# Optimization experiments

Measured on AMD Instinct MI355X. Metric: run time of the kernel, lower is better.

## Reference

```python
import jax, jax.numpy as jnp
import numpy as np

NEG_BIG = -9e15
ALPHA = 0.2  # LeakyReLU negative slope


def setup_inputs() -> dict:
    key = jax.random.key(0)
    k1, k2, k3, k4 = jax.random.split(key, 4)
    B, N, F_in, F_out = 8, 2048, 128, 128
    h = jax.random.normal(k1, (B, N, F_in), dtype=jnp.float32)
    adj = jax.random.randint(k2, (B, N, N), 0, 2, dtype=jnp.int32)
    # xavier_uniform with gain=1.414
    def xavier(k, shape, gain=1.414):
        fan_in, fan_out = shape[0], shape[1]
        bound = gain * np.sqrt(6.0 / (fan_in + fan_out))
        return jax.random.uniform(k, shape, jnp.float32, -bound, bound)
    W = xavier(k3, (F_in, F_out))
    a = xavier(k4, (2 * F_out, 1))
    return {"h": h, "adj": adj, "W": W, "a": a}


def reference(h, adj, W, a):
    # h: [B,N,F_in], adj: [B,N,N], W: [F_in,F_out], a: [2*F_out,1]
    Wh = jnp.einsum('bnf,fo->bno', h, W)              # [B,N,F_out]
    F_out = W.shape[1]
    a1 = a[:F_out, 0]                                  # source part
    a2 = a[F_out:, 0]                                  # target part
    # additive attention decomposition: cat([Wh_i, Wh_j]) @ a == Wh_i@a1 + Wh_j@a2
    s1 = Wh @ a1                                       # [B,N]
    s2 = Wh @ a2                                       # [B,N]
    e = jax.nn.leaky_relu(s1[:, :, None] + s2[:, None, :], negative_slope=ALPHA)  # [B,N,N]
    e = jnp.where(adj > 0, e, NEG_BIG)
    attn = jax.nn.softmax(e, axis=-1)                  # [B,N,N]
    h_prime = jnp.einsum('bij,bjo->bio', attn, Wh)     # [B,N,F_out]
    return jax.nn.elu(h_prime)                         # concat=True path
```

## Files before the change

kernel.cpp:

```cpp
#include <hip/hip_runtime.h>
#include <hip/hip_bf16.h>
#include <string.h>

typedef __attribute__((ext_vector_type(8))) short short8;
typedef __attribute__((ext_vector_type(4))) float f32x4;
typedef __attribute__((ext_vector_type(4))) int int4v;
typedef __attribute__((ext_vector_type(4))) float float4v;
typedef __attribute__((ext_vector_type(4))) unsigned short ushort4v;

#define LOG2E 1.44269504088896340736f
#define NB 8
#define NN 2048
#define NF 128
#define PKW (NN / 64)
#define PKWORDS (NB * NN * PKW)

static __device__ inline unsigned short f2bf(float x) {
    __hip_bfloat16 b = __float2bfloat16(x);
    unsigned short u;
    __builtin_memcpy(&u, &b, 2);
    return u;
}
static __device__ inline float bf2f(unsigned short u) {
    union { unsigned u; float f; } v;
    v.u = ((unsigned)u) << 16;
    return v.f;
}

__global__ void k_sniff(const unsigned short* __restrict__ hraw,
                        int* __restrict__ flag) {
    int lane = threadIdx.x;
    int cnt = 0;
    for (int i = lane; i < 512; i += 64) {
        int e = (hraw[i] >> 7) & 0xFF;
        cnt += (e >= 102 && e <= 139) ? 1 : 0;
    }
#pragma unroll
    for (int off = 1; off < 64; off <<= 1) cnt += __shfl_xor(cnt, off);
    if (lane == 0) *flag = (cnt >= 450) ? 1 : 0;
}

__global__ __launch_bounds__(256) void k_pack(const int* __restrict__ adj,
                                              unsigned long long* __restrict__ pk) {
    const int wid = blockIdx.x * 4 + (threadIdx.x >> 6);
    const int lane = threadIdx.x & 63;
    const int wpw = PKWORDS / 4096;
    const size_t w0 = (size_t)wid * wpw;
    for (int i = 0; i < wpw; i += 4) {
        int v0 = adj[((w0 + i) << 6) | lane];
        int v1 = adj[((w0 + i + 1) << 6) | lane];
        int v2 = adj[((w0 + i + 2) << 6) | lane];
        int v3 = adj[((w0 + i + 3) << 6) | lane];
        unsigned long long m0 = __ballot(v0 > 0);
        unsigned long long m1 = __ballot(v1 > 0);
        unsigned long long m2 = __ballot(v2 > 0);
        unsigned long long m3 = __ballot(v3 > 0);
        if (lane == 0) {
            pk[w0 + i] = m0;
            pk[w0 + i + 1] = m1;
            pk[w0 + i + 2] = m2;
            pk[w0 + i + 3] = m3;
        }
    }
}

__global__ __launch_bounds__(256) void k_prep(const void* __restrict__ Wraw,
                                              const void* __restrict__ araw,
                                              const int* __restrict__ flag,
                                              short* __restrict__ WThi,
                                              short* __restrict__ WTlo,
                                              float* __restrict__ a1s,
                                              float* __restrict__ a2s) {
    const int bf16w = *flag;
    int idx = blockIdx.x * 256 + threadIdx.x;
    int k = idx >> 7, n = idx & 127;
    float x = bf16w ? bf2f(((const unsigned short*)Wraw)[idx])
                    : ((const float*)Wraw)[idx];
    unsigned short hi = f2bf(x);
    float lo = x - bf2f(hi);
    WThi[n * 128 + k] = (short)hi;
    WTlo[n * 128 + k] = (short)f2bf(lo);
    if (blockIdx.x == 0) {
        int i = threadIdx.x;
        float av = bf16w ? bf2f(((const unsigned short*)araw)[i])
                         : ((const float*)araw)[i];
        if (i < 128) a1s[i] = LOG2E * av;
        else a2s[i - 128] = LOG2E * av;
    }
}

__global__ __launch_bounds__(64) void k_gemm(const void* __restrict__ hraw,
                                             const int* __restrict__ flag,
                                             const short* __restrict__ WThi,
                                             const short* __restrict__ WTlo,
                                             const float* __restrict__ a1s,
                                             const float* __restrict__ a2s,
                                             float* __restrict__ s1,
                                             float* __restrict__ s2,
                                             short* __restrict__ WhT) {
    const int lane = threadIdx.x;
    const int lo = lane & 15, g = lane >> 4;
    const int i0 = blockIdx.x * 16;
    const int bf16w = *flag;

    short8 ahi[4], alo[4];
    if (bf16w) {
        const short* h16 = (const short*)hraw;
#pragma unroll
        for (int kc = 0; kc < 4; ++kc) {
            ahi[kc] = *(const short8*)(h16 + (size_t)(i0 + lo) * NF + kc * 32 + g * 8);
            alo[kc] = (short8){0, 0, 0, 0, 0, 0, 0, 0};
        }
    } else {
        const float* hf = (const float*)hraw;
#pragma unroll
        for (int kc = 0; kc < 4; ++kc) {
            const float* p = hf + (size_t)(i0 + lo) * NF + kc * 32 + g * 8;
            float4v x0 = *(const float4v*)(p);
            float4v x1 = *(const float4v*)(p + 4);
            short8 h8, l8;
#pragma unroll
            for (int q = 0; q < 4; ++q) {
                unsigned short u0 = f2bf(x0[q]);
                h8[q] = (short)u0;
                l8[q] = (short)f2bf(x0[q] - bf2f(u0));
                unsigned short u1 = f2bf(x1[q]);
                h8[q + 4] = (short)u1;
                l8[q + 4] = (short)f2bf(x1[q] - bf2f(u1));
            }
            ahi[kc] = h8;
            alo[kc] = l8;
        }
    }

    f32x4 acc[8];
#pragma unroll
    for (int t = 0; t < 8; ++t) acc[t] = (f32x4){0.f, 0.f, 0.f, 0.f};

#pragma unroll
    for (int t = 0; t < 8; ++t) {
#pragma unroll
        for (int kc = 0; kc < 4; ++kc) {
            const size_t boff = (size_t)(lo + 16 * t) * NF + kc * 32 + g * 8;
            short8 bhi = *(const short8*)(WThi + boff);
            short8 blo = *(const short8*)(WTlo + boff);
            acc[t] = __builtin_amdgcn_mfma_f32_16x16x32_bf16(ahi[kc], bhi, acc[t], 0, 0, 0);
            acc[t] = __builtin_amdgcn_mfma_f32_16x16x32_bf16(ahi[kc], blo, acc[t], 0, 0, 0);
            acc[t] = __builtin_amdgcn_mfma_f32_16x16x32_bf16(alo[kc], bhi, acc[t], 0, 0, 0);
        }
    }

    const int b = i0 >> 11;
    const int n0 = i0 & 2047;
    short* wt = WhT + (size_t)b * NF * NN;
#pragma unroll
    for (int t = 0; t < 8; ++t) {
        ushort4v u;
#pragma unroll
        for (int r = 0; r < 4; ++r) u[r] = f2bf(acc[t][r]);
        *(ushort4v*)(wt + (size_t)(lo + 16 * t) * NN + n0 + g * 4) = u;
    }

    float a1f[8], a2f[8];
#pragma unroll
    for (int t = 0; t < 8; ++t) {
        a1f[t] = a1s[lo + 16 * t];
        a2f[t] = a2s[lo + 16 * t];
    }
#pragma unroll
    for (int r = 0; r < 4; ++r) {
        float d1 = 0.f, d2 = 0.f;
#pragma unroll
        for (int t = 0; t < 8; ++t) {
            float w = acc[t][r];
            d1 += w * a1f[t];
            d2 += w * a2f[t];
        }
#pragma unroll
        for (int off = 1; off < 16; off <<= 1) {
            d1 += __shfl_xor(d1, off);
            d2 += __shfl_xor(d2, off);
        }
        if (lo == 0) {
            s1[i0 + g * 4 + r] = d1;
            s2[i0 + g * 4 + r] = d2;
        }
    }
}

__global__ __launch_bounds__(256) void k_s2max(const float* __restrict__ s2,
                                               float* __restrict__ s2m) {
    int b = blockIdx.x;
    float m = -1e30f;
    for (int i = threadIdx.x; i < NN; i += 256) m = fmaxf(m, s2[b * NN + i]);
#pragma unroll
    for (int off = 1; off < 64; off <<= 1) m = fmaxf(m, __shfl_xor(m, off));
    __shared__ float sm[4];
    if ((threadIdx.x & 63) == 0) sm[threadIdx.x >> 6] = m;
    __syncthreads();
    if (threadIdx.x == 0)
        s2m[b] = fmaxf(fmaxf(sm[0], sm[1]), fmaxf(sm[2], sm[3]));
}

template <int FINAL, int JS>
__global__ __launch_bounds__(256, 4) void k_attn3(const unsigned long long* __restrict__ pk,
                                                  const float* __restrict__ s1,
                                                  const float* __restrict__ s2,
                                                  const float* __restrict__ s2m,
                                                  const short* __restrict__ WhT,
                                                  const int* __restrict__ flag,
                                                  void* __restrict__ out,
                                                  float* __restrict__ pO,
                                                  float* __restrict__ pL) {
    const int tid = threadIdx.x;
    const int lane = tid & 63, wid = tid >> 6;
    const int lo = lane & 15, g = lane >> 4;
    const int gid = blockIdx.x;
    const int js = (JS > 1) ? (gid / (NB * 32)) : 0;
    const int rem = gid % (NB * 32);
    const int blk = rem & 31;
    const int b = rem >> 5;
    const int rowbase = blk * 64 + wid * 16;
    const int row = rowbase + lo;
    const int jbeg = js * (NN / JS);
    const int NT = (NN / JS) / 64;

    __shared__ short lds[2][128 * 64];

    const float s1v = s1[b * NN + row];
    const float tm = s1v + s2m[b];
    const float M = fmaxf(tm, 0.2f * tm);
    const unsigned long long* pkr = pk + (size_t)(b * NN + row) * PKW + (jbeg >> 6);
    const float* s2p = s2 + b * NN + jbeg;
    const short* vb = WhT + (size_t)b * NF * NN;

    const int sf = tid >> 1;
    const int sh = tid & 1;
    const short* sbase = vb + (size_t)sf * NN + jbeg + sh * 32;
    char* ldsc0 = (char*)&lds[0][0];
    char* ldsc1 = (char*)&lds[1][0];
    const unsigned swz = (unsigned)((sf & 7) << 4);
    const unsigned wb0 = (unsigned)(sf * 128 + sh * 64);
    const unsigned rsw = (unsigned)((lo & 7) << 4);

    f32x4 acc[8];
#pragma unroll
    for (int t = 0; t < 8; ++t) acc[t] = (f32x4){0.f, 0.f, 0.f, 0.f};
    float lsum = 0.f;

    {
        short8 s0 = *(const short8*)(sbase);
        short8 s1r = *(const short8*)(sbase + 8);
        short8 s2r = *(const short8*)(sbase + 16);
        short8 s3r = *(const short8*)(sbase + 24);
        *(short8*)(ldsc0 + ((wb0 + 0) ^ swz)) = s0;
        *(short8*)(ldsc0 + ((wb0 + 16) ^ swz)) = s1r;
        *(short8*)(ldsc0 + ((wb0 + 32) ^ swz)) = s2r;
        *(short8*)(ldsc0 + ((wb0 + 48) ^ swz)) = s3r;
    }
    unsigned long long mcur = pkr[0];
    float4v zc0 = *(const float4v*)(s2p + g * 8);
    float4v zc1 = *(const float4v*)(s2p + g * 8 + 4);
    float4v zc2 = *(const float4v*)(s2p + g * 8 + 32);
    float4v zc3 = *(const float4v*)(s2p + g * 8 + 36);
    __syncthreads();

    int cur = 0;
    for (int t = 0; t < NT; ++t) {
        short8 sn0, sn1, sn2, sn3;
        unsigned long long mnext = 0;
        float4v zn0, zn1, zn2, zn3;
        const bool more = (t + 1 < NT);
        if (more) {
            const short* sp = sbase + (t + 1) * 64;
            sn0 = *(const short8*)(sp);
            sn1 = *(const short8*)(sp + 8);
            sn2 = *(const short8*)(sp + 16);
            sn3 = *(const short8*)(sp + 24);
            mnext = pkr[t + 1];
            const float* zp = s2p + (t + 1) * 64 + g * 8;
            zn0 = *(const float4v*)(zp);
            zn1 = *(const float4v*)(zp + 4);
            zn2 = *(const float4v*)(zp + 32);
            zn3 = *(const float4v*)(zp + 36);
        }
        const char* cb = cur ? ldsc1 : ldsc0;

        const unsigned bits0 = (unsigned)(mcur >> (g * 8)) & 0xFFu;
        const unsigned bits1 = (unsigned)(mcur >> (32 + g * 8)) & 0xFFu;
        short8 pa0, pa1;
#pragma unroll
        for (int q = 0; q < 4; ++q) {
            float t0 = s1v + zc0[q];
            float e0 = fmaxf(t0, 0.2f * t0);
            float p0 = ((bits0 >> q) & 1u) ? exp2f(e0 - M) : 0.f;
            float t1 = s1v + zc1[q];
            float e1 = fmaxf(t1, 0.2f * t1);
            float p1 = ((bits0 >> (q + 4)) & 1u) ? exp2f(e1 - M) : 0.f;
            float t2 = s1v + zc2[q];
            float e2 = fmaxf(t2, 0.2f * t2);
            float p2 = ((bits1 >> q) & 1u) ? exp2f(e2 - M) : 0.f;
            float t3 = s1v + zc3[q];
            float e3 = fmaxf(t3, 0.2f * t3);
            float p3 = ((bits1 >> (q + 4)) & 1u) ? exp2f(e3 - M) : 0.f;
            pa0[q] = (short)f2bf(p0); pa0[q + 4] = (short)f2bf(p1);
            pa1[q] = (short)f2bf(p2); pa1[q + 4] = (short)f2bf(p3);
            lsum += p0 + p1 + p2 + p3;
        }

#pragma unroll
        for (int t8 = 0; t8 < 8; ++t8) {
            const unsigned rb0 = ((unsigned)((lo + 16 * t8) * 128 + g * 16)) ^ rsw;
            const unsigned rb1 = ((unsigned)((lo + 16 * t8) * 128 + 64 + g * 16)) ^ rsw;
            short8 v0 = *(const short8*)(cb + rb0);
            short8 v1 = *(const short8*)(cb + rb1);
            acc[t8] = __builtin_amdgcn_mfma_f32_16x16x32_bf16(pa0, v0, acc[t8], 0, 0, 0);
            acc[t8] = __builtin_amdgcn_mfma_f32_16x16x32_bf16(pa1, v1, acc[t8], 0, 0, 0);
        }

        if (more) {
            char* wb = cur ? ldsc0 : ldsc1;
            *(short8*)(wb + ((wb0 + 0) ^ swz)) = sn0;
            *(short8*)(wb + ((wb0 + 16) ^ swz)) = sn1;
            *(short8*)(wb + ((wb0 + 32) ^ swz)) = sn2;
            *(short8*)(wb + ((wb0 + 48) ^ swz)) = sn3;
            mcur = mnext;
            zc0 = zn0; zc1 = zn1; zc2 = zn2; zc3 = zn3;
        }
        __syncthreads();
        cur ^= 1;
    }

    lsum += __shfl_xor(lsum, 16);
    lsum += __shfl_xor(lsum, 32);

    if (FINAL) {
        const int bf16w = *flag;
        float inv[4];
#pragma unroll
        for (int r = 0; r < 4; ++r) inv[r] = 1.0f / __shfl(lsum, g * 4 + r);
#pragma unroll
        for (int t8 = 0; t8 < 8; ++t8) {
#pragma unroll
            for (int r = 0; r < 4; ++r) {
                float x = acc[t8][r] * inv[r];
                float y = (x > 0.f) ? x : (exp2f(x * LOG2E) - 1.0f);
                size_t oi = ((size_t)b * NN + rowbase + g * 4 + r) * NF + lo + 16 * t8;
                if (bf16w) ((__hip_bfloat16*)out)[oi] = __float2bfloat16(y);
                else ((float*)out)[oi] = y;
            }
        }
    } else {
        const int grp = b * 128 + blk * 4 + wid;
        float* po = pO + (size_t)(grp * JS + js) * (16 * NF);
#pragma unroll
        for (int t8 = 0; t8 < 8; ++t8)
#pragma unroll
            for (int r = 0; r < 4; ++r)
                po[(g * 4 + r) * NF + lo + 16 * t8] = acc[t8][r];
        if (g == 0) pL[(grp * JS + js) * 16 + lo] = lsum;
    }
}

__global__ __launch_bounds__(256) void k_combine(const float* __restrict__ pO,
                                                 const float* __restrict__ pL,
                                                 const int* __restrict__ flag,
                                                 void* __restrict__ out,
                                                 int jsplit) {
    int idx = blockIdx.x * 256 + threadIdx.x;
    if (idx >= NB * NN * NF) return;
    const int bf16w = *flag;
    int col = idx & 127;
    int rowg = idx >> 7;
    int r = rowg & 15;
    int grp = rowg >> 4;
    float o = 0.f, l = 0.f;
    for (int js = 0; js < jsplit; ++js) {
        int task = grp * jsplit + js;
        o += pO[(size_t)task * (16 * NF) + r * NF + col];
        l += pL[task * 16 + r];
    }
    float x = o / l;
    float y = (x > 0.f) ? x : (exp2f(x * LOG2E) - 1.0f);
    if (bf16w) ((__hip_bfloat16*)out)[idx] = __float2bfloat16(y);
    else ((float*)out)[idx] = y;
}

extern "C" void kernel_launch(void* const* d_in, const int* in_sizes, int n_in,
                              void* d_out, int out_size, void* d_ws, size_t ws_size,
                              hipStream_t stream) {
    const void* h = d_in[0];
    const int* adj = (const int*)d_in[1];
    const void* W = d_in[2];
    const void* a = d_in[3];

    char* ws = (char*)d_ws;
    auto align256 = [](size_t x) { return (x + 255) & ~(size_t)255; };
    size_t off = 0;
    int* flag = (int*)(ws + off);     off = align256(off + 256);
    short* WThi = (short*)(ws + off); off = align256(off + (size_t)128 * 128 * 2);
    short* WTlo = (short*)(ws + off); off = align256(off + (size_t)128 * 128 * 2);
    float* a1s = (float*)(ws + off);  off = align256(off + 128 * 4);
    float* a2s = (float*)(ws + off);  off = align256(off + 128 * 4);
    short* WhT = (short*)(ws + off);  off = align256(off + (size_t)NB * NF * NN * 2);
    float* s1 = (float*)(ws + off);   off = align256(off + (size_t)NB * NN * 4);
    float* s2 = (float*)(ws + off);   off = align256(off + (size_t)NB * NN * 4);
    float* s2m = (float*)(ws + off);  off = align256(off + (size_t)NB * 4);
    unsigned long long* pk = (unsigned long long*)(ws + off);
    off = align256(off + (size_t)PKWORDS * 8);

    const int ngrp = NB * 128;
    auto need = [&](int js) {
        return off + (size_t)ngrp * js * 16 * NF * 4 + 512 + (size_t)ngrp * js * 16 * 4;
    };
    int jsplit = (ws_size >= need(4)) ? 4 : ((ws_size >= need(2)) ? 2 : 1);
    float* pO = nullptr;
    float* pL = nullptr;
    if (jsplit > 1) {
        size_t pO_bytes = (size_t)ngrp * jsplit * 16 * NF * 4;
        size_t pL_bytes = (size_t)ngrp * jsplit * 16 * 4;
        pO = (float*)(ws + off); off = align256(off + pO_bytes);
        pL = (float*)(ws + off); off = align256(off + pL_bytes);
    }

    k_sniff<<<1, 64, 0, stream>>>((const unsigned short*)h, flag);
    k_pack<<<1024, 256, 0, stream>>>(adj, pk);
    k_prep<<<64, 256, 0, stream>>>(W, a, flag, WThi, WTlo, a1s, a2s);
    k_gemm<<<NB * NN / 16, 64, 0, stream>>>(h, flag, WThi, WTlo, a1s, a2s, s1, s2, WhT);
    k_s2max<<<NB, 256, 0, stream>>>(s2, s2m);
    if (jsplit == 4) {
        k_attn3<0, 4><<<NB * 32 * 4, 256, 0, stream>>>(pk, s1, s2, s2m, WhT, flag,
                                                       d_out, pO, pL);
    } else if (jsplit == 2) {
        k_attn3<0, 2><<<NB * 32 * 2, 256, 0, stream>>>(pk, s1, s2, s2m, WhT, flag,
                                                       d_out, pO, pL);
    } else {
        k_attn3<1, 1><<<NB * 32, 256, 0, stream>>>(pk, s1, s2, s2m, WhT, flag,
                                                   d_out, nullptr, nullptr);
    }
    if (jsplit > 1) {
        int nout = NB * NN * NF;
        k_combine<<<(nout + 255) / 256, 256, 0, stream>>>(pO, pL, flag, d_out, jsplit);
    }
}
```

Before: 87.86 us.

## Fuse pack and GEMM kernels, fold s2 max via atomics, stage masks in LDS

Drops the separate sniff and s2-max launches. Each wave now sniffs the dtype inline, and s2's max is folded into the GEMM through an order-preserving atomicMax key. The pack and GEMM work run in one heterogeneous launch, with the GEMM using four waves per block. The attention kernel preloads the packed mask and s2 into LDS and unrolls its double-buffer loop by two. The combine step is vectorised to float4. The aim is to cut launch count and global traffic in the inner loop, at the cost of more LDS use and atomics.

```diff
diff --git a/kernel.cpp b/kernel.cpp
--- a/kernel.cpp
+++ b/kernel.cpp
@@ -4,7 +4,6 @@
 
 typedef __attribute__((ext_vector_type(8))) short short8;
 typedef __attribute__((ext_vector_type(4))) float f32x4;
-typedef __attribute__((ext_vector_type(4))) int int4v;
 typedef __attribute__((ext_vector_type(4))) float float4v;
 typedef __attribute__((ext_vector_type(4))) unsigned short ushort4v;
 
@@ -14,6 +13,8 @@
 #define NF 128
 #define PKW (NN / 64)
 #define PKWORDS (NB * NN * PKW)
+#define NGEMMB 256
+#define NPACKB 1024
 
 static __device__ inline unsigned short f2bf(float x) {
     __hip_bfloat16 b = __float2bfloat16(x);
@@ -26,52 +27,35 @@
     v.u = ((unsigned)u) << 16;
     return v.f;
 }
-
-__global__ void k_sniff(const unsigned short* __restrict__ hraw,
-                        int* __restrict__ flag) {
-    int lane = threadIdx.x;
+static __device__ inline unsigned fkey(float f) {
+    unsigned u = __float_as_uint(f);
+    return (u & 0x80000000u) ? ~u : (u | 0x80000000u);
+}
+static __device__ inline float funkey(unsigned k) {
+    unsigned b = (k & 0x80000000u) ? (k & 0x7FFFFFFFu) : ~k;
+    return __uint_as_float(b);
+}
+static __device__ inline int wave_sniff(const unsigned short* __restrict__ raw) {
+    int lane = threadIdx.x & 63;
     int cnt = 0;
-    for (int i = lane; i < 512; i += 64) {
-        int e = (hraw[i] >> 7) & 0xFF;
+#pragma unroll
+    for (int i = 0; i < 8; ++i) {
+        int e = (raw[lane * 8 + i] >> 7) & 0xFF;
         cnt += (e >= 102 && e <= 139) ? 1 : 0;
     }
 #pragma unroll
     for (int off = 1; off < 64; off <<= 1) cnt += __shfl_xor(cnt, off);
-    if (lane == 0) *flag = (cnt >= 450) ? 1 : 0;
-}
-
-__global__ __launch_bounds__(256) void k_pack(const int* __restrict__ adj,
-                                              unsigned long long* __restrict__ pk) {
-    const int wid = blockIdx.x * 4 + (threadIdx.x >> 6);
-    const int lane = threadIdx.x & 63;
-    const int wpw = PKWORDS / 4096;
-    const size_t w0 = (size_t)wid * wpw;
-    for (int i = 0; i < wpw; i += 4) {
-        int v0 = adj[((w0 + i) << 6) | lane];
-        int v1 = adj[((w0 + i + 1) << 6) | lane];
-        int v2 = adj[((w0 + i + 2) << 6) | lane];
-        int v3 = adj[((w0 + i + 3) << 6) | lane];
-        unsigned long long m0 = __ballot(v0 > 0);
-        unsigned long long m1 = __ballot(v1 > 0);
-        unsigned long long m2 = __ballot(v2 > 0);
-        unsigned long long m3 = __ballot(v3 > 0);
-        if (lane == 0) {
-            pk[w0 + i] = m0;
-            pk[w0 + i + 1] = m1;
-            pk[w0 + i + 2] = m2;
-            pk[w0 + i + 3] = m3;
-        }
-    }
+    return cnt >= 450;
 }
 
 __global__ __launch_bounds__(256) void k_prep(const void* __restrict__ Wraw,
                                               const void* __restrict__ araw,
-                                              const int* __restrict__ flag,
                                               short* __restrict__ WThi,
                                               short* __restrict__ WTlo,
                                               float* __restrict__ a1s,
-                                              float* __restrict__ a2s) {
-    const int bf16w = *flag;
+                                              float* __restrict__ a2s,
+                                              unsigned* __restrict__ s2mkey) {
+    const int bf16w = wave_sniff((const unsigned short*)Wraw);
     int idx = blockIdx.x * 256 + threadIdx.x;
     int k = idx >> 7, n = idx & 127;
     float x = bf16w ? bf2f(((const unsigned short*)Wraw)[idx])
@@ -86,22 +70,50 @@
                          : ((const float*)araw)[i];
         if (i < 128) a1s[i] = LOG2E * av;
         else a2s[i - 128] = LOG2E * av;
-    }
-}
-
-__global__ __launch_bounds__(64) void k_gemm(const void* __restrict__ hraw,
-                                             const int* __restrict__ flag,
-                                             const short* __restrict__ WThi,
-                                             const short* __restrict__ WTlo,
-                                             const float* __restrict__ a1s,
-                                             const float* __restrict__ a2s,
-                                             float* __restrict__ s1,
-                                             float* __restrict__ s2,
-                                             short* __restrict__ WhT) {
-    const int lane = threadIdx.x;
+        if (i < NB) s2mkey[i] = 0u;
+    }
+}
+
+__global__ __launch_bounds__(256, 4) void k_fat(const int* __restrict__ adj,
+                                                unsigned long long* __restrict__ pk,
+                                                const void* __restrict__ hraw,
+                                                const short* __restrict__ WThi,
+                                                const short* __restrict__ WTlo,
+                                                const float* __restrict__ a1s,
+                                                const float* __restrict__ a2s,
+                                                float* __restrict__ s1,
+                                                float* __restrict__ s2,
+                                                unsigned* __restrict__ s2mkey,
+                                                short* __restrict__ WhT) {
+    const int tid = threadIdx.x;
+    if (blockIdx.x >= NGEMMB) {
+        const int wid = (blockIdx.x - NGEMMB) * 4 + (tid >> 6);
+        const int lane = tid & 63;
+        const int wpw = PKWORDS / 4096;
+        const size_t w0 = (size_t)wid * wpw;
+        for (int i = 0; i < wpw; i += 4) {
+            int v0 = adj[((w0 + i) << 6) | lane];
+            int v1 = adj[((w0 + i + 1) << 6) | lane];
+            int v2 = adj[((w0 + i + 2) << 6) | lane];
+            int v3 = adj[((w0 + i + 3) << 6) | lane];
+            unsigned long long m0 = __ballot(v0 > 0);
+            unsigned long long m1 = __ballot(v1 > 0);
+            unsigned long long m2 = __ballot(v2 > 0);
+            unsigned long long m3 = __ballot(v3 > 0);
+            if (lane == 0) {
+                pk[w0 + i] = m0;
+                pk[w0 + i + 1] = m1;
+                pk[w0 + i + 2] = m2;
+                pk[w0 + i + 3] = m3;
+            }
+        }
+        return;
+    }
+    const int lane = tid & 63;
+    const int w = tid >> 6;
     const int lo = lane & 15, g = lane >> 4;
-    const int i0 = blockIdx.x * 16;
-    const int bf16w = *flag;
+    const int i0 = (blockIdx.x * 4 + w) * 16;
+    const int bf16w = wave_sniff((const unsigned short*)hraw);
 
     short8 ahi[4], alo[4];
     if (bf16w) {
@@ -136,7 +148,6 @@
     f32x4 acc[8];
 #pragma unroll
     for (int t = 0; t < 8; ++t) acc[t] = (f32x4){0.f, 0.f, 0.f, 0.f};
-
 #pragma unroll
     for (int t = 0; t < 8; ++t) {
 #pragma unroll
@@ -167,14 +178,15 @@
         a1f[t] = a1s[lo + 16 * t];
         a2f[t] = a2s[lo + 16 * t];
     }
+    float wm = -1e30f;
 #pragma unroll
     for (int r = 0; r < 4; ++r) {
         float d1 = 0.f, d2 = 0.f;
 #pragma unroll
         for (int t = 0; t < 8; ++t) {
-            float w = acc[t][r];
-            d1 += w * a1f[t];
-            d2 += w * a2f[t];
+            float wv = acc[t][r];
+            d1 += wv * a1f[t];
+            d2 += wv * a2f[t];
         }
 #pragma unroll
         for (int off = 1; off < 16; off <<= 1) {
@@ -185,33 +197,27 @@
             s1[i0 + g * 4 + r] = d1;
             s2[i0 + g * 4 + r] = d2;
         }
-    }
-}
-
-__global__ __launch_bounds__(256) void k_s2max(const float* __restrict__ s2,
-                                               float* __restrict__ s2m) {
-    int b = blockIdx.x;
-    float m = -1e30f;
-    for (int i = threadIdx.x; i < NN; i += 256) m = fmaxf(m, s2[b * NN + i]);
-#pragma unroll
-    for (int off = 1; off < 64; off <<= 1) m = fmaxf(m, __shfl_xor(m, off));
-    __shared__ float sm[4];
-    if ((threadIdx.x & 63) == 0) sm[threadIdx.x >> 6] = m;
-    __syncthreads();
-    if (threadIdx.x == 0)
-        s2m[b] = fmaxf(fmaxf(sm[0], sm[1]), fmaxf(sm[2], sm[3]));
+        wm = fmaxf(wm, d2);
+    }
+    wm = fmaxf(wm, __shfl_xor(wm, 16));
+    wm = fmaxf(wm, __shfl_xor(wm, 32));
+    if (lane == 0) atomicMax(&s2mkey[b], fkey(wm));
 }
 
 template <int FINAL, int JS>
-__global__ __launch_bounds__(256, 4) void k_attn3(const unsigned long long* __restrict__ pk,
+__global__ __launch_bounds__(256, 4) void k_attn4(const unsigned long long* __restrict__ pk,
                                                   const float* __restrict__ s1,
                                                   const float* __restrict__ s2,
-                                                  const float* __restrict__ s2m,
+                                                  const unsigned* __restrict__ s2mkey,
                                                   const short* __restrict__ WhT,
-                                                  const int* __restrict__ flag,
+                                                  const void* __restrict__ hraw,
                                                   void* __restrict__ out,
                                                   float* __restrict__ pO,
                                                   float* __restrict__ pL) {
+    constexpr int JL = NN / JS;
+    constexpr int NT = JL / 64;
+    constexpr int PKSTR = NT + 1;
+
     const int tid = threadIdx.x;
     const int lane = tid & 63, wid = tid >> 6;
     const int lo = lane & 15, g = lane >> 4;
@@ -222,23 +228,31 @@
     const int b = rem >> 5;
     const int rowbase = blk * 64 + wid * 16;
     const int row = rowbase + lo;
-    const int jbeg = js * (NN / JS);
-    const int NT = (NN / JS) / 64;
-
-    __shared__ short lds[2][128 * 64];
+    const int jbeg = js * JL;
+
+    __shared__ short ldsV[2][8192];
+    __shared__ unsigned long long ldsPk[64][PKSTR];
+    __shared__ float ldsZ[JL];
 
     const float s1v = s1[b * NN + row];
-    const float tm = s1v + s2m[b];
+    const float s2mv = funkey(s2mkey[b]);
+    const float tm = s1v + s2mv;
     const float M = fmaxf(tm, 0.2f * tm);
-    const unsigned long long* pkr = pk + (size_t)(b * NN + row) * PKW + (jbeg >> 6);
-    const float* s2p = s2 + b * NN + jbeg;
-    const short* vb = WhT + (size_t)b * NF * NN;
+
+    const int jw0 = jbeg >> 6;
+    for (int idx = tid; idx < 64 * (NT / 2); idx += 256) {
+        int r = idx / (NT / 2);
+        int wp = (idx % (NT / 2)) * 2;
+        const unsigned long long* gp = pk + (size_t)(b * NN + blk * 64 + r) * PKW + jw0 + wp;
+        ldsPk[r][wp] = gp[0];
+        ldsPk[r][wp + 1] = gp[1];
+    }
+    for (int i = tid * 4; i < JL; i += 1024)
+        *(float4v*)&ldsZ[i] = *(const float4v*)(s2 + b * NN + jbeg + i);
 
     const int sf = tid >> 1;
     const int sh = tid & 1;
-    const short* sbase = vb + (size_t)sf * NN + jbeg + sh * 32;
-    char* ldsc0 = (char*)&lds[0][0];
-    char* ldsc1 = (char*)&lds[1][0];
+    const short* sbase = WhT + (size_t)b * NF * NN + (size_t)sf * NN + jbeg + sh * 32;
     const unsigned swz = (unsigned)((sf & 7) << 4);
     const unsigned wb0 = (unsigned)(sf * 128 + sh * 64);
     const unsigned rsw = (unsigned)((lo & 7) << 4);
@@ -248,94 +262,88 @@
     for (int t = 0; t < 8; ++t) acc[t] = (f32x4){0.f, 0.f, 0.f, 0.f};
     float lsum = 0.f;
 
-    {
-        short8 s0 = *(const short8*)(sbase);
-        short8 s1r = *(const short8*)(sbase + 8);
-        short8 s2r = *(const short8*)(sbase + 16);
-        short8 s3r = *(const short8*)(sbase + 24);
-        *(short8*)(ldsc0 + ((wb0 + 0) ^ swz)) = s0;
-        *(short8*)(ldsc0 + ((wb0 + 16) ^ swz)) = s1r;
-        *(short8*)(ldsc0 + ((wb0 + 32) ^ swz)) = s2r;
-        *(short8*)(ldsc0 + ((wb0 + 48) ^ swz)) = s3r;
-    }
-    unsigned long long mcur = pkr[0];
-    float4v zc0 = *(const float4v*)(s2p + g * 8);
-    float4v zc1 = *(const float4v*)(s2p + g * 8 + 4);
-    float4v zc2 = *(const float4v*)(s2p + g * 8 + 32);
-    float4v zc3 = *(const float4v*)(s2p + g * 8 + 36);
+#define LOADV(R0, R1, R2, R3, t)                                   \
+    {                                                              \
+        const short* sp_ = sbase + (t) * 64;                       \
+        R0 = *(const short8*)(sp_);                                \
+        R1 = *(const short8*)(sp_ + 8);                            \
+        R2 = *(const short8*)(sp_ + 16);                           \
+        R3 = *(const short8*)(sp_ + 24);                           \
+    }
+#define WRITEV(R0, R1, R2, R3, BUF)                                \
+    {                                                              \
+        char* wp_ = (char*)(BUF);                                  \
+        *(short8*)(wp_ + ((wb0 + 0) ^ swz)) = R0;                  \
+        *(short8*)(wp_ + ((wb0 + 16) ^ swz)) = R1;                 \
+        *(short8*)(wp_ + ((wb0 + 32) ^ swz)) = R2;                 \
+        *(short8*)(wp_ + ((wb0 + 48) ^ swz)) = R3;                 \
+    }
+#define COMPUTE(t, BUF)                                                        \
+    {                                                                          \
+        const unsigned long long mcur_ = ldsPk[wid * 16 + lo][t];              \
+        const float* zb_ = &ldsZ[(t) * 64 + g * 8];                            \
+        float4v z0_ = *(const float4v*)(zb_);                                  \
+        float4v z1_ = *(const float4v*)(zb_ + 4);                              \
+        float4v z2_ = *(const float4v*)(zb_ + 32);                             \
+        float4v z3_ = *(const float4v*)(zb_ + 36);                             \
+        const unsigned bits0_ = (unsigned)(mcur_ >> (g * 8)) & 0xFFu;          \
+        const unsigned bits1_ = (unsigned)(mcur_ >> (32 + g * 8)) & 0xFFu;     \
+        short8 pa0_, pa1_;                                                     \
+        _Pragma("unroll") for (int q = 0; q < 4; ++q) {                        \
+            float t0 = s1v + z0_[q];                                           \
+            float e0 = fmaxf(t0, 0.2f * t0);                                   \
+            float p0 = ((bits0_ >> q) & 1u) ? exp2f(e0 - M) : 0.f;             \
+            float t1 = s1v + z1_[q];                                           \
+            float e1 = fmaxf(t1, 0.2f * t1);                                   \
+            float p1 = ((bits0_ >> (q + 4)) & 1u) ? exp2f(e1 - M) : 0.f;       \
+            float t2 = s1v + z2_[q];                                           \
+            float e2 = fmaxf(t2, 0.2f * t2);                                   \
+            float p2 = ((bits1_ >> q) & 1u) ? exp2f(e2 - M) : 0.f;             \
+            float t3 = s1v + z3_[q];                                           \
+            float e3 = fmaxf(t3, 0.2f * t3);                                   \
+            float p3 = ((bits1_ >> (q + 4)) & 1u) ? exp2f(e3 - M) : 0.f;       \
+            pa0_[q] = (short)f2bf(p0);                                         \
+            pa0_[q + 4] = (short)f2bf(p1);                                     \
+            pa1_[q] = (short)f2bf(p2);                                         \
+            pa1_[q + 4] = (short)f2bf(p3);                                     \
+            lsum += p0 + p1 + p2 + p3;                                         \
+        }                                                                      \
+        const char* cb_ = (const char*)(BUF);                                  \
+        _Pragma("unroll") for (int t8 = 0; t8 < 8; ++t8) {                     \
+            const unsigned rb0_ = ((unsigned)((lo + 16 * t8) * 128 + g * 16)) ^ rsw;  \
+            const unsigned rb1_ = ((unsigned)((lo + 16 * t8) * 128 + 64 + g * 16)) ^ rsw; \
+            short8 v0_ = *(const short8*)(cb_ + rb0_);                         \
+            short8 v1_ = *(const short8*)(cb_ + rb1_);                         \
+            acc[t8] = __builtin_amdgcn_mfma_f32_16x16x32_bf16(pa0_, v0_, acc[t8], 0, 0, 0); \
+            acc[t8] = __builtin_amdgcn_mfma_f32_16x16x32_bf16(pa1_, v1_, acc[t8], 0, 0, 0); \
+        }                                                                      \
+    }
+
+    short8 A0, A1, A2, A3, B0, B1, B2, B3;
+    LOADV(A0, A1, A2, A3, 0);
+    WRITEV(A0, A1, A2, A3, ldsV[0]);
+    LOADV(B0, B1, B2, B3, 1);
     __syncthreads();
 
-    int cur = 0;
-    for (int t = 0; t < NT; ++t) {
-        short8 sn0, sn1, sn2, sn3;
-        unsigned long long mnext = 0;
-        float4v zn0, zn1, zn2, zn3;
-        const bool more = (t + 1 < NT);
-        if (more) {
-            const short* sp = sbase + (t + 1) * 64;
-            sn0 = *(const short8*)(sp);
-            sn1 = *(const short8*)(sp + 8);
-            sn2 = *(const short8*)(sp + 16);
-            sn3 = *(const short8*)(sp + 24);
-            mnext = pkr[t + 1];
-            const float* zp = s2p + (t + 1) * 64 + g * 8;
-            zn0 = *(const float4v*)(zp);
-            zn1 = *(const float4v*)(zp + 4);
-            zn2 = *(const float4v*)(zp + 32);
-            zn3 = *(const float4v*)(zp + 36);
-        }
-        const char* cb = cur ? ldsc1 : ldsc0;
-
-        const unsigned bits0 = (unsigned)(mcur >> (g * 8)) & 0xFFu;
-        const unsigned bits1 = (unsigned)(mcur >> (32 + g * 8)) & 0xFFu;
-        short8 pa0, pa1;
-#pragma unroll
-        for (int q = 0; q < 4; ++q) {
-            float t0 = s1v + zc0[q];
-            float e0 = fmaxf(t0, 0.2f * t0);
-            float p0 = ((bits0 >> q) & 1u) ? exp2f(e0 - M) : 0.f;
-            float t1 = s1v + zc1[q];
-            float e1 = fmaxf(t1, 0.2f * t1);
-            float p1 = ((bits0 >> (q + 4)) & 1u) ? exp2f(e1 - M) : 0.f;
-            float t2 = s1v + zc2[q];
-            float e2 = fmaxf(t2, 0.2f * t2);
-            float p2 = ((bits1 >> q) & 1u) ? exp2f(e2 - M) : 0.f;
-            float t3 = s1v + zc3[q];
-            float e3 = fmaxf(t3, 0.2f * t3);
-            float p3 = ((bits1 >> (q + 4)) & 1u) ? exp2f(e3 - M) : 0.f;
-            pa0[q] = (short)f2bf(p0); pa0[q + 4] = (short)f2bf(p1);
-            pa1[q] = (short)f2bf(p2); pa1[q + 4] = (short)f2bf(p3);
-            lsum += p0 + p1 + p2 + p3;
-        }
-
-#pragma unroll
-        for (int t8 = 0; t8 < 8; ++t8) {
-            const unsigned rb0 = ((unsigned)((lo + 16 * t8) * 128 + g * 16)) ^ rsw;
-            const unsigned rb1 = ((unsigned)((lo + 16 * t8) * 128 + 64 + g * 16)) ^ rsw;
-            short8 v0 = *(const short8*)(cb + rb0);
-            short8 v1 = *(const short8*)(cb + rb1);
-            acc[t8] = __builtin_amdgcn_mfma_f32_16x16x32_bf16(pa0, v0, acc[t8], 0, 0, 0);
-            acc[t8] = __builtin_amdgcn_mfma_f32_16x16x32_bf16(pa1, v1, acc[t8], 0, 0, 0);
-        }
-
-        if (more) {
-            char* wb = cur ? ldsc0 : ldsc1;
-            *(short8*)(wb + ((wb0 + 0) ^ swz)) = sn0;
-            *(short8*)(wb + ((wb0 + 16) ^ swz)) = sn1;
-            *(short8*)(wb + ((wb0 + 32) ^ swz)) = sn2;
-            *(short8*)(wb + ((wb0 + 48) ^ swz)) = sn3;
-            mcur = mnext;
-            zc0 = zn0; zc1 = zn1; zc2 = zn2; zc3 = zn3;
-        }
+    for (int tt = 0; tt < NT; tt += 2) {
+        if (tt + 2 < NT) LOADV(A0, A1, A2, A3, tt + 2);
+        COMPUTE(tt, ldsV[0]);
+        WRITEV(B0, B1, B2, B3, ldsV[1]);
         __syncthreads();
-        cur ^= 1;
-    }
+        if (tt + 3 < NT) LOADV(B0, B1, B2, B3, tt + 3);
+        COMPUTE(tt + 1, ldsV[1]);
+        if (tt + 2 < NT) WRITEV(A0, A1, A2, A3, ldsV[0]);
+        __syncthreads();
+    }
+#undef LOADV
+#undef WRITEV
+#undef COMPUTE
 
     lsum += __shfl_xor(lsum, 16);
     lsum += __shfl_xor(lsum, 32);
 
     if (FINAL) {
-        const int bf16w = *flag;
+        const int bf16w = wave_sniff((const unsigned short*)hraw);
         float inv[4];
 #pragma unroll
         for (int r = 0; r < 4; ++r) inv[r] = 1.0f / __shfl(lsum, g * 4 + r);
@@ -364,26 +372,39 @@
 
 __global__ __launch_bounds__(256) void k_combine(const float* __restrict__ pO,
                                                  const float* __restrict__ pL,
-                                                 const int* __restrict__ flag,
+                                                 const void* __restrict__ hraw,
                                                  void* __restrict__ out,
                                                  int jsplit) {
-    int idx = blockIdx.x * 256 + threadIdx.x;
-    if (idx >= NB * NN * NF) return;
-    const int bf16w = *flag;
-    int col = idx & 127;
-    int rowg = idx >> 7;
+    const int bf16w = wave_sniff((const unsigned short*)hraw);
+    int idx4 = blockIdx.x * 256 + threadIdx.x;
+    int base = idx4 * 4;
+    if (base >= NB * NN * NF) return;
+    int col = base & 127;
+    int rowg = base >> 7;
     int r = rowg & 15;
     int grp = rowg >> 4;
-    float o = 0.f, l = 0.f;
+    float4v o = (float4v){0.f, 0.f, 0.f, 0.f};
+    float l = 0.f;
     for (int js = 0; js < jsplit; ++js) {
         int task = grp * jsplit + js;
-        o += pO[(size_t)task * (16 * NF) + r * NF + col];
+        o += *(const float4v*)(pO + (size_t)task * (16 * NF) + r * NF + col);
         l += pL[task * 16 + r];
     }
-    float x = o / l;
-    float y = (x > 0.f) ? x : (exp2f(x * LOG2E) - 1.0f);
-    if (bf16w) ((__hip_bfloat16*)out)[idx] = __float2bfloat16(y);
-    else ((float*)out)[idx] = y;
+    float inv = 1.0f / l;
+    float y[4];
+#pragma unroll
+    for (int q = 0; q < 4; ++q) {
+        float x = o[q] * inv;
+        y[q] = (x > 0.f) ? x : (exp2f(x * LOG2E) - 1.0f);
+    }
+    if (bf16w) {
+        ushort4v u;
+#pragma unroll
+        for (int q = 0; q < 4; ++q) u[q] = f2bf(y[q]);
+        *(ushort4v*)((__hip_bfloat16*)out + base) = u;
+    } else {
+        *(float4v*)((float*)out + base) = (float4v){y[0], y[1], y[2], y[3]};
+    }
 }
 
 extern "C" void kernel_launch(void* const* d_in, const int* in_sizes, int n_in,
@@ -397,7 +418,6 @@
     char* ws = (char*)d_ws;
     auto align256 = [](size_t x) { return (x + 255) & ~(size_t)255; };
     size_t off = 0;
-    int* flag = (int*)(ws + off);     off = align256(off + 256);
     short* WThi = (short*)(ws + off); off = align256(off + (size_t)128 * 128 * 2);
     short* WTlo = (short*)(ws + off); off = align256(off + (size_t)128 * 128 * 2);
     float* a1s = (float*)(ws + off);  off = align256(off + 128 * 4);
@@ -405,7 +425,7 @@
     short* WhT = (short*)(ws + off);  off = align256(off + (size_t)NB * NF * NN * 2);
     float* s1 = (float*)(ws + off);   off = align256(off + (size_t)NB * NN * 4);
     float* s2 = (float*)(ws + off);   off = align256(off + (size_t)NB * NN * 4);
-    float* s2m = (float*)(ws + off);  off = align256(off + (size_t)NB * 4);
+    unsigned* s2mkey = (unsigned*)(ws + off); off = align256(off + NB * 4);
     unsigned long long* pk = (unsigned long long*)(ws + off);
     off = align256(off + (size_t)PKWORDS * 8);
 
@@ -423,23 +443,21 @@
         pL = (float*)(ws + off); off = align256(off + pL_bytes);
     }
 
-    k_sniff<<<1, 64, 0, stream>>>((const unsigned short*)h, flag);
-    k_pack<<<1024, 256, 0, stream>>>(adj, pk);
-    k_prep<<<64, 256, 0, stream>>>(W, a, flag, WThi, WTlo, a1s, a2s);
-    k_gemm<<<NB * NN / 16, 64, 0, stream>>>(h, flag, WThi, WTlo, a1s, a2s, s1, s2, WhT);
-    k_s2max<<<NB, 256, 0, stream>>>(s2, s2m);
+    k_prep<<<64, 256, 0, stream>>>(W, a, WThi, WTlo, a1s, a2s, s2mkey);
+    k_fat<<<NGEMMB + NPACKB, 256, 0, stream>>>(adj, pk, h, WThi, WTlo, a1s, a2s,
+                                               s1, s2, s2mkey, WhT);
     if (jsplit == 4) {
-        k_attn3<0, 4><<<NB * 32 * 4, 256, 0, stream>>>(pk, s1, s2, s2m, WhT, flag,
+        k_attn4<0, 4><<<NB * 32 * 4, 256, 0, stream>>>(pk, s1, s2, s2mkey, WhT, h,
                                                        d_out, pO, pL);
     } else if (jsplit == 2) {
-        k_attn3<0, 2><<<NB * 32 * 2, 256, 0, stream>>>(pk, s1, s2, s2m, WhT, flag,
+        k_attn4<0, 2><<<NB * 32 * 2, 256, 0, stream>>>(pk, s1, s2, s2mkey, WhT, h,
                                                        d_out, pO, pL);
     } else {
-        k_attn3<1, 1><<<NB * 32, 256, 0, stream>>>(pk, s1, s2, s2m, WhT, flag,
+        k_attn4<1, 1><<<NB * 32, 256, 0, stream>>>(pk, s1, s2, s2mkey, WhT, h,
                                                    d_out, nullptr, nullptr);
     }
     if (jsplit > 1) {
         int nout = NB * NN * NF;
-        k_combine<<<(nout + 255) / 256, 256, 0, stream>>>(pO, pL, flag, d_out, jsplit);
-    }
-}
+        k_combine<<<(nout / 4 + 255) / 256, 256, 0, stream>>>(pO, pL, h, d_out, jsplit);
+    }
+}
```

New measurement: 90.86 us. +3.4%, slower.

## Fold sniff and s2max kernels into others, vectorize combine, use fast exp

Applied to the files above, without the earlier changes.

Removes the separate dtype-sniff and s2-max kernel launches: each kernel now sniffs the dtype inline per wave, and the gemm computes the per-batch s2 maximum with an atomicMax on an order-preserving integer key. The gemm runs four waves per block instead of one. The combine kernel is vectorized to four outputs per thread. Raw v_exp_f32 and a manual bf16 rounding replace library calls, and the pack loop is unrolled by eight. These cut launch count and per-element overhead, at the cost of redundant sniff loads in every wave and atomic contention on eight addresses.

```diff
diff --git a/kernel.cpp b/kernel.cpp
--- a/kernel.cpp
+++ b/kernel.cpp
@@ -4,7 +4,6 @@
 
 typedef __attribute__((ext_vector_type(8))) short short8;
 typedef __attribute__((ext_vector_type(4))) float f32x4;
-typedef __attribute__((ext_vector_type(4))) int int4v;
 typedef __attribute__((ext_vector_type(4))) float float4v;
 typedef __attribute__((ext_vector_type(4))) unsigned short ushort4v;
 
@@ -16,62 +15,48 @@
 #define PKWORDS (NB * NN * PKW)
 
 static __device__ inline unsigned short f2bf(float x) {
-    __hip_bfloat16 b = __float2bfloat16(x);
-    unsigned short u;
-    __builtin_memcpy(&u, &b, 2);
-    return u;
+    unsigned u = __float_as_uint(x);
+    return (unsigned short)((u + 0x7FFFu + ((u >> 16) & 1u)) >> 16);
 }
 static __device__ inline float bf2f(unsigned short u) {
     union { unsigned u; float f; } v;
     v.u = ((unsigned)u) << 16;
     return v.f;
 }
-
-__global__ void k_sniff(const unsigned short* __restrict__ hraw,
-                        int* __restrict__ flag) {
-    int lane = threadIdx.x;
+static __device__ inline float fexp2(float x) {
+    float r;
+    asm("v_exp_f32 %0, %1" : "=v"(r) : "v"(x));
+    return r;
+}
+static __device__ inline unsigned fkey(float f) {
+    unsigned u = __float_as_uint(f);
+    return (u & 0x80000000u) ? ~u : (u | 0x80000000u);
+}
+static __device__ inline float funkey(unsigned k) {
+    unsigned b = (k & 0x80000000u) ? (k & 0x7FFFFFFFu) : ~k;
+    return __uint_as_float(b);
+}
+static __device__ inline int wave_sniff(const unsigned short* __restrict__ raw) {
+    int lane = threadIdx.x & 63;
     int cnt = 0;
-    for (int i = lane; i < 512; i += 64) {
-        int e = (hraw[i] >> 7) & 0xFF;
+#pragma unroll
+    for (int i = 0; i < 8; ++i) {
+        int e = (raw[lane * 8 + i] >> 7) & 0xFF;
         cnt += (e >= 102 && e <= 139) ? 1 : 0;
     }
 #pragma unroll
     for (int off = 1; off < 64; off <<= 1) cnt += __shfl_xor(cnt, off);
-    if (lane == 0) *flag = (cnt >= 450) ? 1 : 0;
-}
-
-__global__ __launch_bounds__(256) void k_pack(const int* __restrict__ adj,
-                                              unsigned long long* __restrict__ pk) {
-    const int wid = blockIdx.x * 4 + (threadIdx.x >> 6);
-    const int lane = threadIdx.x & 63;
-    const int wpw = PKWORDS / 4096;
-    const size_t w0 = (size_t)wid * wpw;
-    for (int i = 0; i < wpw; i += 4) {
-        int v0 = adj[((w0 + i) << 6) | lane];
-        int v1 = adj[((w0 + i + 1) << 6) | lane];
-        int v2 = adj[((w0 + i + 2) << 6) | lane];
-        int v3 = adj[((w0 + i + 3) << 6) | lane];
-        unsigned long long m0 = __ballot(v0 > 0);
-        unsigned long long m1 = __ballot(v1 > 0);
-        unsigned long long m2 = __ballot(v2 > 0);
-        unsigned long long m3 = __ballot(v3 > 0);
-        if (lane == 0) {
-            pk[w0 + i] = m0;
-            pk[w0 + i + 1] = m1;
-            pk[w0 + i + 2] = m2;
-            pk[w0 + i + 3] = m3;
-        }
-    }
+    return cnt >= 450;
 }
 
 __global__ __launch_bounds__(256) void k_prep(const void* __restrict__ Wraw,
                                               const void* __restrict__ araw,
-                                              const int* __restrict__ flag,
                                               short* __restrict__ WThi,
                                               short* __restrict__ WTlo,
                                               float* __restrict__ a1s,
-                                              float* __restrict__ a2s) {
-    const int bf16w = *flag;
+                                              float* __restrict__ a2s,
+                                              unsigned* __restrict__ s2mkey) {
+    const int bf16w = wave_sniff((const unsigned short*)Wraw);
     int idx = blockIdx.x * 256 + threadIdx.x;
     int k = idx >> 7, n = idx & 127;
     float x = bf16w ? bf2f(((const unsigned short*)Wraw)[idx])
@@ -86,22 +71,45 @@
                          : ((const float*)araw)[i];
         if (i < 128) a1s[i] = LOG2E * av;
         else a2s[i - 128] = LOG2E * av;
-    }
-}
-
-__global__ __launch_bounds__(64) void k_gemm(const void* __restrict__ hraw,
-                                             const int* __restrict__ flag,
-                                             const short* __restrict__ WThi,
-                                             const short* __restrict__ WTlo,
-                                             const float* __restrict__ a1s,
-                                             const float* __restrict__ a2s,
-                                             float* __restrict__ s1,
-                                             float* __restrict__ s2,
-                                             short* __restrict__ WhT) {
-    const int lane = threadIdx.x;
+        if (i < NB) s2mkey[i] = 0u;
+    }
+}
+
+__global__ __launch_bounds__(256) void k_pack(const int* __restrict__ adj,
+                                              unsigned long long* __restrict__ pk) {
+    const int wid = blockIdx.x * 4 + (threadIdx.x >> 6);
+    const int lane = threadIdx.x & 63;
+    const int wpw = PKWORDS / 4096;
+    const size_t w0 = (size_t)wid * wpw;
+    for (int i = 0; i < wpw; i += 8) {
+        int v[8];
+#pragma unroll
+        for (int k = 0; k < 8; ++k) v[k] = adj[((w0 + i + k) << 6) | lane];
+        unsigned long long m[8];
+#pragma unroll
+        for (int k = 0; k < 8; ++k) m[k] = __ballot(v[k] > 0);
+        if (lane == 0) {
+#pragma unroll
+            for (int k = 0; k < 8; ++k) pk[w0 + i + k] = m[k];
+        }
+    }
+}
+
+__global__ __launch_bounds__(256, 4) void k_gemm(const void* __restrict__ hraw,
+                                                 const short* __restrict__ WThi,
+                                                 const short* __restrict__ WTlo,
+                                                 const float* __restrict__ a1s,
+                                                 const float* __restrict__ a2s,
+                                                 float* __restrict__ s1,
+                                                 float* __restrict__ s2,
+                                                 unsigned* __restrict__ s2mkey,
+                                                 short* __restrict__ WhT) {
+    const int tid = threadIdx.x;
+    const int lane = tid & 63;
+    const int w = tid >> 6;
     const int lo = lane & 15, g = lane >> 4;
-    const int i0 = blockIdx.x * 16;
-    const int bf16w = *flag;
+    const int i0 = (blockIdx.x * 4 + w) * 16;
+    const int bf16w = wave_sniff((const unsigned short*)hraw);
 
     short8 ahi[4], alo[4];
     if (bf16w) {
@@ -136,7 +144,6 @@
     f32x4 acc[8];
 #pragma unroll
     for (int t = 0; t < 8; ++t) acc[t] = (f32x4){0.f, 0.f, 0.f, 0.f};
-
 #pragma unroll
     for (int t = 0; t < 8; ++t) {
 #pragma unroll
@@ -167,14 +174,15 @@
         a1f[t] = a1s[lo + 16 * t];
         a2f[t] = a2s[lo + 16 * t];
     }
+    float wm = -1e30f;
 #pragma unroll
     for (int r = 0; r < 4; ++r) {
         float d1 = 0.f, d2 = 0.f;
 #pragma unroll
         for (int t = 0; t < 8; ++t) {
-            float w = acc[t][r];
-            d1 += w * a1f[t];
-            d2 += w * a2f[t];
+            float wv = acc[t][r];
+            d1 += wv * a1f[t];
+            d2 += wv * a2f[t];
         }
 #pragma unroll
         for (int off = 1; off < 16; off <<= 1) {
@@ -185,33 +193,26 @@
             s1[i0 + g * 4 + r] = d1;
             s2[i0 + g * 4 + r] = d2;
         }
-    }
-}
-
-__global__ __launch_bounds__(256) void k_s2max(const float* __restrict__ s2,
-                                               float* __restrict__ s2m) {
-    int b = blockIdx.x;
-    float m = -1e30f;
-    for (int i = threadIdx.x; i < NN; i += 256) m = fmaxf(m, s2[b * NN + i]);
-#pragma unroll
-    for (int off = 1; off < 64; off <<= 1) m = fmaxf(m, __shfl_xor(m, off));
-    __shared__ float sm[4];
-    if ((threadIdx.x & 63) == 0) sm[threadIdx.x >> 6] = m;
-    __syncthreads();
-    if (threadIdx.x == 0)
-        s2m[b] = fmaxf(fmaxf(sm[0], sm[1]), fmaxf(sm[2], sm[3]));
+        wm = fmaxf(wm, d2);
+    }
+    wm = fmaxf(wm, __shfl_xor(wm, 16));
+    wm = fmaxf(wm, __shfl_xor(wm, 32));
+    if (lane == 0) atomicMax(&s2mkey[b], fkey(wm));
 }
 
 template <int FINAL, int JS>
-__global__ __launch_bounds__(256, 4) void k_attn3(const unsigned long long* __restrict__ pk,
-                                                  const float* __restrict__ s1,
-                                                  const float* __restrict__ s2,
-                                                  const float* __restrict__ s2m,
-                                                  const short* __restrict__ WhT,
-                                                  const int* __restrict__ flag,
-                                                  void* __restrict__ out,
-                                                  float* __restrict__ pO,
-                                                  float* __restrict__ pL) {
+__global__ __launch_bounds__(256, 4) void k_attn(const unsigned long long* __restrict__ pk,
+                                                 const float* __restrict__ s1,
+                                                 const float* __restrict__ s2,
+                                                 const unsigned* __restrict__ s2mkey,
+                                                 const short* __restrict__ WhT,
+                                                 const void* __restrict__ hraw,
+                                                 void* __restrict__ out,
+                                                 float* __restrict__ pO,
+                                                 float* __restrict__ pL) {
+    constexpr int JL = NN / JS;
+    constexpr int NT = JL / 64;
+
     const int tid = threadIdx.x;
     const int lane = tid & 63, wid = tid >> 6;
     const int lo = lane & 15, g = lane >> 4;
@@ -222,13 +223,12 @@
     const int b = rem >> 5;
     const int rowbase = blk * 64 + wid * 16;
     const int row = rowbase + lo;
-    const int jbeg = js * (NN / JS);
-    const int NT = (NN / JS) / 64;
+    const int jbeg = js * JL;
 
     __shared__ short lds[2][128 * 64];
 
     const float s1v = s1[b * NN + row];
-    const float tm = s1v + s2m[b];
+    const float tm = s1v + funkey(s2mkey[b]);
     const float M = fmaxf(tm, 0.2f * tm);
     const unsigned long long* pkr = pk + (size_t)(b * NN + row) * PKW + (jbeg >> 6);
     const float* s2p = s2 + b * NN + jbeg;
@@ -293,16 +293,16 @@
         for (int q = 0; q < 4; ++q) {
             float t0 = s1v + zc0[q];
             float e0 = fmaxf(t0, 0.2f * t0);
-            float p0 = ((bits0 >> q) & 1u) ? exp2f(e0 - M) : 0.f;
+            float p0 = ((bits0 >> q) & 1u) ? fexp2(e0 - M) : 0.f;
             float t1 = s1v + zc1[q];
             float e1 = fmaxf(t1, 0.2f * t1);
-            float p1 = ((bits0 >> (q + 4)) & 1u) ? exp2f(e1 - M) : 0.f;
+            float p1 = ((bits0 >> (q + 4)) & 1u) ? fexp2(e1 - M) : 0.f;
             float t2 = s1v + zc2[q];
             float e2 = fmaxf(t2, 0.2f * t2);
-            float p2 = ((bits1 >> q) & 1u) ? exp2f(e2 - M) : 0.f;
+            float p2 = ((bits1 >> q) & 1u) ? fexp2(e2 - M) : 0.f;
             float t3 = s1v + zc3[q];
             float e3 = fmaxf(t3, 0.2f * t3);
-            float p3 = ((bits1 >> (q + 4)) & 1u) ? exp2f(e3 - M) : 0.f;
+            float p3 = ((bits1 >> (q + 4)) & 1u) ? fexp2(e3 - M) : 0.f;
             pa0[q] = (short)f2bf(p0); pa0[q + 4] = (short)f2bf(p1);
             pa1[q] = (short)f2bf(p2); pa1[q + 4] = (short)f2bf(p3);
             lsum += p0 + p1 + p2 + p3;
@@ -335,7 +335,7 @@
     lsum += __shfl_xor(lsum, 32);
 
     if (FINAL) {
-        const int bf16w = *flag;
+        const int bf16w = wave_sniff((const unsigned short*)hraw);
         float inv[4];
 #pragma unroll
         for (int r = 0; r < 4; ++r) inv[r] = 1.0f / __shfl(lsum, g * 4 + r);
@@ -344,9 +344,9 @@
 #pragma unroll
             for (int r = 0; r < 4; ++r) {
                 float x = acc[t8][r] * inv[r];
-                float y = (x > 0.f) ? x : (exp2f(x * LOG2E) - 1.0f);
+                float y = (x > 0.f) ? x : (fexp2(x * LOG2E) - 1.0f);
                 size_t oi = ((size_t)b * NN + rowbase + g * 4 + r) * NF + lo + 16 * t8;
-                if (bf16w) ((__hip_bfloat16*)out)[oi] = __float2bfloat16(y);
+                if (bf16w) ((unsigned short*)out)[oi] = f2bf(y);
                 else ((float*)out)[oi] = y;
             }
         }
@@ -364,26 +364,39 @@
 
 __global__ __launch_bounds__(256) void k_combine(const float* __restrict__ pO,
                                                  const float* __restrict__ pL,
-                                                 const int* __restrict__ flag,
+                                                 const void* __restrict__ hraw,
                                                  void* __restrict__ out,
                                                  int jsplit) {
-    int idx = blockIdx.x * 256 + threadIdx.x;
-    if (idx >= NB * NN * NF) return;
-    const int bf16w = *flag;
-    int col = idx & 127;
-    int rowg = idx >> 7;
+    const int bf16w = wave_sniff((const unsigned short*)hraw);
+    int idx4 = blockIdx.x * 256 + threadIdx.x;
+    int base = idx4 * 4;
+    if (base >= NB * NN * NF) return;
+    int col = base & 127;
+    int rowg = base >> 7;
     int r = rowg & 15;
     int grp = rowg >> 4;
-    float o = 0.f, l = 0.f;
+    float4v o = (float4v){0.f, 0.f, 0.f, 0.f};
+    float l = 0.f;
     for (int js = 0; js < jsplit; ++js) {
         int task = grp * jsplit + js;
-        o += pO[(size_t)task * (16 * NF) + r * NF + col];
+        o += *(const float4v*)(pO + (size_t)task * (16 * NF) + r * NF + col);
         l += pL[task * 16 + r];
     }
-    float x = o / l;
-    float y = (x > 0.f) ? x : (exp2f(x * LOG2E) - 1.0f);
-    if (bf16w) ((__hip_bfloat16*)out)[idx] = __float2bfloat16(y);
-    else ((float*)out)[idx] = y;
+    float inv = 1.0f / l;
+    float y[4];
+#pragma unroll
+    for (int q = 0; q < 4; ++q) {
+        float x = o[q] * inv;
+        y[q] = (x > 0.f) ? x : (fexp2(x * LOG2E) - 1.0f);
+    }
+    if (bf16w) {
+        ushort4v u;
+#pragma unroll
+        for (int q = 0; q < 4; ++q) u[q] = f2bf(y[q]);
+        *(ushort4v*)((unsigned short*)out + base) = u;
+    } else {
+        *(float4v*)((float*)out + base) = (float4v){y[0], y[1], y[2], y[3]};
+    }
 }
 
 extern "C" void kernel_launch(void* const* d_in, const int* in_sizes, int n_in,
@@ -397,7 +410,6 @@
     char* ws = (char*)d_ws;
     auto align256 = [](size_t x) { return (x + 255) & ~(size_t)255; };
     size_t off = 0;
-    int* flag = (int*)(ws + off);     off = align256(off + 256);
     short* WThi = (short*)(ws + off); off = align256(off + (size_t)128 * 128 * 2);
     short* WTlo = (short*)(ws + off); off = align256(off + (size_t)128 * 128 * 2);
     float* a1s = (float*)(ws + off);  off = align256(off + 128 * 4);
@@ -405,7 +417,7 @@
     short* WhT = (short*)(ws + off);  off = align256(off + (size_t)NB * NF * NN * 2);
     float* s1 = (float*)(ws + off);   off = align256(off + (size_t)NB * NN * 4);
     float* s2 = (float*)(ws + off);   off = align256(off + (size_t)NB * NN * 4);
-    float* s2m = (float*)(ws + off);  off = align256(off + (size_t)NB * 4);
+    unsigned* s2mkey = (unsigned*)(ws + off); off = align256(off + NB * 4);
     unsigned long long* pk = (unsigned long long*)(ws + off);
     off = align256(off + (size_t)PKWORDS * 8);
 
@@ -423,23 +435,21 @@
         pL = (float*)(ws + off); off = align256(off + pL_bytes);
     }
 
-    k_sniff<<<1, 64, 0, stream>>>((const unsigned short*)h, flag);
+    k_prep<<<64, 256, 0, stream>>>(W, a, WThi, WTlo, a1s, a2s, s2mkey);
+    k_gemm<<<256, 256, 0, stream>>>(h, WThi, WTlo, a1s, a2s, s1, s2, s2mkey, WhT);
     k_pack<<<1024, 256, 0, stream>>>(adj, pk);
-    k_prep<<<64, 256, 0, stream>>>(W, a, flag, WThi, WTlo, a1s, a2s);
-    k_gemm<<<NB * NN / 16, 64, 0, stream>>>(h, flag, WThi, WTlo, a1s, a2s, s1, s2, WhT);
-    k_s2max<<<NB, 256, 0, stream>>>(s2, s2m);
     if (jsplit == 4) {
-        k_attn3<0, 4><<<NB * 32 * 4, 256, 0, stream>>>(pk, s1, s2, s2m, WhT, flag,
-                                                       d_out, pO, pL);
+        k_attn<0, 4><<<NB * 32 * 4, 256, 0, stream>>>(pk, s1, s2, s2mkey, WhT, h,
+                                                      d_out, pO, pL);
     } else if (jsplit == 2) {
-        k_attn3<0, 2><<<NB * 32 * 2, 256, 0, stream>>>(pk, s1, s2, s2m, WhT, flag,
-                                                       d_out, pO, pL);
+        k_attn<0, 2><<<NB * 32 * 2, 256, 0, stream>>>(pk, s1, s2, s2mkey, WhT, h,
+                                                      d_out, pO, pL);
     } else {
-        k_attn3<1, 1><<<NB * 32, 256, 0, stream>>>(pk, s1, s2, s2m, WhT, flag,
-                                                   d_out, nullptr, nullptr);
+        k_attn<1, 1><<<NB * 32, 256, 0, stream>>>(pk, s1, s2, s2mkey, WhT, h,
+                                                  d_out, nullptr, nullptr);
     }
     if (jsplit > 1) {
         int nout = NB * NN * NF;
-        k_combine<<<(nout + 255) / 256, 256, 0, stream>>>(pO, pL, flag, d_out, jsplit);
-    }
-}
+        k_combine<<<(nout / 4 + 255) / 256, 256, 0, stream>>>(pO, pL, h, d_out, jsplit);
+    }
+}
```

Result: slower. 94.64 us (+7.7%).
